# Kernel tuning notes

Hardware: AMD Instinct MI355X
Metric: run time of the kernel (lower is better)

Reference implementation:

```python
import jax, jax.numpy as jnp
import numpy as np

B, L, D = 2, 2048, 2048
H, HKV, HD = 32, 8, 64
G = H // HKV  # GQA group size


def _rope(t, cos, sin):
    # t: [B, h, L, HD]; cos/sin: [L, HD//2]; pairs are consecutive (view_as_complex)
    tr, ti = t[..., 0::2], t[..., 1::2]
    out_r = tr * cos - ti * sin
    out_i = tr * sin + ti * cos
    return jnp.stack([out_r, out_i], axis=-1).reshape(t.shape)


def setup_inputs() -> dict:
    key = jax.random.key(0)
    ks = jax.random.split(key, 5)
    x = jax.random.normal(ks[0], (B, L, D), dtype=jnp.float32)
    wq = jax.random.normal(ks[1], (D, H * HD), dtype=jnp.float32) * 0.02
    wk = jax.random.normal(ks[2], (D, HKV * HD), dtype=jnp.float32) * 0.02
    wv = jax.random.normal(ks[3], (D, HKV * HD), dtype=jnp.float32) * 0.02
    wo = jax.random.normal(ks[4], (D, D), dtype=jnp.float32) * 0.02
    # RoPE freqs: theta_i = 10000^(-2i/HD), angle[p, i] = p * theta_i
    inv_freq = 1.0 / (10000.0 ** (jnp.arange(0, HD, 2, dtype=jnp.float32) / HD))
    angles = jnp.arange(L, dtype=jnp.float32)[:, None] * inv_freq[None, :]  # [L, HD//2]
    freqs_cos = jnp.cos(angles)
    freqs_sin = jnp.sin(angles)
    # additive causal mask [L, L]
    mask = jnp.where(jnp.tril(jnp.ones((L, L), dtype=bool)), 0.0, -1e9).astype(jnp.float32)
    return {"x": x, "wq": wq, "wk": wk, "wv": wv, "wo": wo,
            "freqs_cos": freqs_cos, "freqs_sin": freqs_sin, "mask": mask}


def reference(x, wq, wk, wv, wo, freqs_cos, freqs_sin, mask):
    b, l, _ = x.shape
    q = (x @ wq).reshape(b, l, H, HD).transpose(0, 2, 1, 3)      # [B, H, L, HD]
    k = (x @ wk).reshape(b, l, HKV, HD).transpose(0, 2, 1, 3)    # [B, HKV, L, HD]
    v = (x @ wv).reshape(b, l, HKV, HD).transpose(0, 2, 1, 3)
    q = _rope(q, freqs_cos, freqs_sin)
    k = _rope(k, freqs_cos, freqs_sin)
    # native GQA broadcast instead of repeat_kv copy (same math)
    qg = q.reshape(b, HKV, G, l, HD)
    scores = jnp.einsum("bhgqd,bhkd->bhgqk", qg, k) / jnp.sqrt(jnp.float32(HD))
    scores = scores + mask  # [B, HKV, G, L, L]
    probs = jax.nn.softmax(scores.astype(jnp.float32), axis=-1).astype(v.dtype)
    out = jnp.einsum("bhgqk,bhkd->bhgqd", probs, v)              # [B, HKV, G, L, HD]
    out = out.reshape(b, H, l, HD).transpose(0, 2, 1, 3).reshape(b, l, H * HD)
    return out @ wo
```

## Files before the change

### kernel.cpp

```cpp
#include <hip/hip_runtime.h>
#include <hip/hip_bf16.h>

#define B_   2
#define L_   2048
#define D_   2048
#define H_   32
#define HKV_ 8
#define HD_  64
#define G_   4
#define M_   4096
#define NF_  3072

typedef __attribute__((ext_vector_type(8))) short bf16x8;
typedef __attribute__((ext_vector_type(4))) float f32x4;

static __device__ __forceinline__ unsigned short f2bf(float f) {
  unsigned int u = __float_as_uint(f);
  unsigned int r = (u + 0x7FFFu + ((u >> 16) & 1u)) >> 16;
  return (unsigned short)r;
}
static __device__ __forceinline__ unsigned short f2bf_hw(float f) {
  __hip_bfloat16 h = __float2bfloat16(f);
  return *(unsigned short*)&h;
}

#define GLD16(g, l) __builtin_amdgcn_global_load_lds(                      \
    (const __attribute__((address_space(1))) void*)(g),                    \
    (__attribute__((address_space(3))) void*)(l), 16, 0, 0)

__global__ void cast_bf16_kernel(const float* __restrict__ in,
                                 unsigned short* __restrict__ out, int n4) {
  int i = blockIdx.x * blockDim.x + threadIdx.x;
  if (i >= n4) return;
  float4 v = ((const float4*)in)[i];
  uint2 r;
  r.x = (unsigned int)f2bf(v.x) | ((unsigned int)f2bf(v.y) << 16);
  r.y = (unsigned int)f2bf(v.z) | ((unsigned int)f2bf(v.w) << 16);
  ((uint2*)out)[i] = r;
}

__global__ void transpose_cast_kernel(const float* __restrict__ src,
                                      unsigned short* __restrict__ dst,
                                      int K, int N) {
  __shared__ float tile[32][33];
  int k0 = blockIdx.y * 32, n0 = blockIdx.x * 32;
  int tx = threadIdx.x, ty = threadIdx.y;
#pragma unroll
  for (int r = 0; r < 4; ++r)
    tile[ty * 4 + r][tx] = src[(size_t)(k0 + ty * 4 + r) * N + n0 + tx];
  __syncthreads();
#pragma unroll
  for (int r = 0; r < 4; ++r)
    dst[(size_t)(n0 + ty * 4 + r) * K + k0 + tx] = f2bf(tile[tx][ty * 4 + r]);
}

__global__ __launch_bounds__(256)
void gemm_bt_kernel(const unsigned short* __restrict__ A,
                    const unsigned short* __restrict__ Bt,
                    float* __restrict__ C, int M, int N, int K) {
  __shared__ unsigned short Al[128 * 32];
  __shared__ unsigned short Bl[128 * 32];
  const int tid = threadIdx.x;
  const int w = tid >> 6;
  const int l = tid & 63;
  const int row0 = blockIdx.y * 128;
  const int col0 = blockIdx.x * 128;
  const int wr = (w >> 1) * 64, wc = (w & 1) * 64;

  f32x4 acc[4][4];
#pragma unroll
  for (int m = 0; m < 4; ++m)
#pragma unroll
    for (int n = 0; n < 4; ++n) acc[m][n] = (f32x4){0.f, 0.f, 0.f, 0.f};

  const int srow = l >> 2;
  const int scol = (l & 3) * 8;
  const int fr = l & 15, fk = (l >> 4) * 8;
  const int nk = K / 32;

  for (int kt = 0; kt < nk; ++kt) {
    const int k0 = kt * 32;
#pragma unroll
    for (int t = 0; t < 2; ++t) {
      const int rr = (w * 2 + t) * 16 + srow;
      GLD16(A + (size_t)(row0 + rr) * K + k0 + scol, &Al[(w * 2 + t) * 512]);
      GLD16(Bt + (size_t)(col0 + rr) * K + k0 + scol, &Bl[(w * 2 + t) * 512]);
    }
    __syncthreads();
    bf16x8 af[4], bfr[4];
#pragma unroll
    for (int m = 0; m < 4; ++m)
      af[m] = *(const bf16x8*)&Al[(wr + m * 16 + fr) * 32 + fk];
#pragma unroll
    for (int n = 0; n < 4; ++n)
      bfr[n] = *(const bf16x8*)&Bl[(wc + n * 16 + fr) * 32 + fk];
#pragma unroll
    for (int m = 0; m < 4; ++m)
#pragma unroll
      for (int n = 0; n < 4; ++n)
        acc[m][n] = __builtin_amdgcn_mfma_f32_16x16x32_bf16(af[m], bfr[n], acc[m][n], 0, 0, 0);
    __syncthreads();
  }

  const int fq = l >> 4;
#pragma unroll
  for (int m = 0; m < 4; ++m)
#pragma unroll
    for (int n = 0; n < 4; ++n)
#pragma unroll
      for (int j = 0; j < 4; ++j) {
        int r = row0 + wr + m * 16 + fq * 4 + j;
        int c = col0 + wc + n * 16 + fr;
        C[(size_t)r * N + c] = acc[m][n][j];
      }
}

__global__ void rope_kernel(const float* __restrict__ src,
                            const float* __restrict__ cosf,
                            const float* __restrict__ sinf,
                            unsigned short* __restrict__ dst, int nh, int col_off,
                            float scale, int total) {
  int idx = blockIdx.x * blockDim.x + threadIdx.x;
  if (idx >= total) return;
  int i = idx & 31;
  int h = (idx >> 5) & (nh - 1);
  int row = idx / (nh << 5);
  int lpos = row & (L_ - 1);
  int b = row >> 11;
  const float* s = src + (size_t)row * NF_ + col_off + h * 64 + 2 * i;
  float tr = s[0], ti = s[1];
  float c = cosf[lpos * 32 + i], sn = sinf[lpos * 32 + i];
  float orr = (tr * c - ti * sn) * scale;
  float oii = (tr * sn + ti * c) * scale;
  size_t o = (((size_t)(b * nh + h)) * L_ + lpos) * 64 + 2 * i;
  unsigned int packed = (unsigned int)f2bf(orr) | ((unsigned int)f2bf(oii) << 16);
  *(unsigned int*)&dst[o] = packed;
}

__global__ void cast_vT_kernel(const float* __restrict__ v,
                               unsigned short* __restrict__ vT) {
  __shared__ float tile[32][33];
  int l0 = blockIdx.x * 32, d0 = blockIdx.y * 32;
  int z = blockIdx.z;
  int b = z >> 3, hkv = z & 7;
  int tx = threadIdx.x, ty = threadIdx.y;
  const float* src = v + (size_t)(b * L_) * NF_ + 2560 + hkv * 64;
#pragma unroll
  for (int r = 0; r < 4; ++r)
    tile[ty * 4 + r][tx] = src[(size_t)(l0 + ty * 4 + r) * NF_ + d0 + tx];
  __syncthreads();
  unsigned short* dst = vT + ((size_t)z * 64) * L_;
#pragma unroll
  for (int r = 0; r < 4; ++r)
    dst[(size_t)(d0 + ty * 4 + r) * L_ + l0 + tx] = f2bf(tile[tx][ty * 4 + r]);
}

__global__ __launch_bounds__(256)
void attn_kernel(const unsigned short* __restrict__ Q,
                 const unsigned short* __restrict__ Kt,
                 const unsigned short* __restrict__ Vt,
                 unsigned short* __restrict__ O) {
  __shared__ unsigned short Kl[64 * 64];
  __shared__ unsigned short Vl[64 * 64];
  __shared__ unsigned short Pl[64 * 64];
  const int tid = threadIdx.x, w = tid >> 6, l = tid & 63;
  const int bh = blockIdx.x;
  const int b = bh >> 5, h = bh & 31;
  const int hkv = h >> 2;
  const int pair = blockIdx.y;
  const int fr = l & 15, hi = l >> 4;
  const int frx = fr & 7;

  const int srow = l >> 3;
  const int scole = ((l & 7) ^ srow) * 8;

  const unsigned short* kbase = Kt + ((size_t)(b * HKV_ + hkv)) * L_ * 64;
  const unsigned short* vbase = Vt + ((size_t)(b * HKV_ + hkv)) * 64 * L_;

  for (int half = 0; half < 2; ++half) {
    const int by = half ? (15 - pair) : pair;
    const int q0 = by * 128;

    bf16x8 qf[2][2];
#pragma unroll
    for (int s = 0; s < 2; ++s) {
      const unsigned short* qb =
          Q + (((size_t)bh) * L_ + q0 + s * 64 + w * 16 + fr) * 64 + hi * 8;
      qf[s][0] = *(const bf16x8*)(qb);
      qf[s][1] = *(const bf16x8*)(qb + 32);
    }

    float m_i[2][4], l_p[2][4];
    f32x4 oacc[2][4];
#pragma unroll
    for (int s = 0; s < 2; ++s)
#pragma unroll
      for (int j = 0; j < 4; ++j) { m_i[s][j] = -1e30f; l_p[s][j] = 0.f; }
#pragma unroll
    for (int s = 0; s < 2; ++s)
#pragma unroll
      for (int nf = 0; nf < 4; ++nf) oacc[s][nf] = (f32x4){0.f, 0.f, 0.f, 0.f};

    const int nt = 2 * by + 2;

    for (int t = 0; t < nt; ++t) {
      const int kv0 = t * 64;
#pragma unroll
      for (int u = 0; u < 2; ++u) {
        const int c = w * 2 + u;
        const int rr = c * 8 + srow;
        GLD16(kbase + ((size_t)(kv0 + rr)) * 64 + scole, &Kl[c * 512]);
        GLD16(vbase + ((size_t)rr) * L_ + kv0 + scole, &Vl[c * 512]);
      }
      __syncthreads();

#pragma unroll
      for (int s = 0; s < 2; ++s) {
        const int dlim = 2 * by + s;
        if (t > dlim) continue;

        f32x4 sacc[4];
#pragma unroll
        for (int nf = 0; nf < 4; ++nf) sacc[nf] = (f32x4){0.f, 0.f, 0.f, 0.f};
#pragma unroll
        for (int ks = 0; ks < 2; ++ks) {
#pragma unroll
          for (int nf = 0; nf < 4; ++nf) {
            bf16x8 kfrag = *(const bf16x8*)
                &Kl[(nf * 16 + fr) * 64 + (((ks * 4 + hi) ^ frx) * 8)];
            sacc[nf] = __builtin_amdgcn_mfma_f32_16x16x32_bf16(qf[s][ks], kfrag, sacc[nf], 0, 0, 0);
          }
        }

        if (t == dlim) {
          const int rbase = q0 + s * 64 + w * 16 + hi * 4;
#pragma unroll
          for (int nf = 0; nf < 4; ++nf)
#pragma unroll
            for (int j = 0; j < 4; ++j)
              if (kv0 + nf * 16 + fr > rbase + j) sacc[nf][j] = -1e30f;
        }

        float rowmax[4];
#pragma unroll
        for (int j = 0; j < 4; ++j) {
          float mx = fmaxf(fmaxf(sacc[0][j], sacc[1][j]),
                           fmaxf(sacc[2][j], sacc[3][j]));
          mx = fmaxf(mx, __shfl_xor(mx, 1));
          mx = fmaxf(mx, __shfl_xor(mx, 2));
          mx = fmaxf(mx, __shfl_xor(mx, 4));
          mx = fmaxf(mx, __shfl_xor(mx, 8));
          rowmax[j] = mx;
        }

        float g = rowmax[0] - m_i[s][0];
        g = fmaxf(g, rowmax[1] - m_i[s][1]);
        g = fmaxf(g, rowmax[2] - m_i[s][2]);
        g = fmaxf(g, rowmax[3] - m_i[s][3]);
        if (!__all(g <= 8.f)) {
#pragma unroll
          for (int j = 0; j < 4; ++j) {
            float mnew = fmaxf(m_i[s][j], rowmax[j]);
            float cr = exp2f(m_i[s][j] - mnew);
            m_i[s][j] = mnew;
            l_p[s][j] *= cr;
#pragma unroll
            for (int nf = 0; nf < 4; ++nf) oacc[s][nf][j] *= cr;
          }
        }

#pragma unroll
        for (int j = 0; j < 4; ++j) {
          const int prow = w * 16 + hi * 4 + j;
#pragma unroll
          for (int nf = 0; nf < 4; ++nf) {
            float p = exp2f(sacc[nf][j] - m_i[s][j]);
            l_p[s][j] += p;
            Pl[prow * 64 + (((nf * 2 + (fr >> 3)) ^ (prow & 7)) * 8) + frx] =
                f2bf_hw(p);
          }
        }

#pragma unroll
        for (int ks = 0; ks < 2; ++ks) {
          bf16x8 pa = *(const bf16x8*)
              &Pl[(w * 16 + fr) * 64 + (((ks * 4 + hi) ^ frx) * 8)];
#pragma unroll
          for (int nf = 0; nf < 4; ++nf) {
            bf16x8 vfrag = *(const bf16x8*)
                &Vl[(nf * 16 + fr) * 64 + (((ks * 4 + hi) ^ frx) * 8)];
            oacc[s][nf] = __builtin_amdgcn_mfma_f32_16x16x32_bf16(pa, vfrag, oacc[s][nf], 0, 0, 0);
          }
        }
      }
      __syncthreads();
    }

#pragma unroll
    for (int s = 0; s < 2; ++s)
#pragma unroll
      for (int j = 0; j < 4; ++j) {
        float lsum = l_p[s][j];
        lsum += __shfl_xor(lsum, 1);
        lsum += __shfl_xor(lsum, 2);
        lsum += __shfl_xor(lsum, 4);
        lsum += __shfl_xor(lsum, 8);
        float inv = 1.0f / lsum;
#pragma unroll
        for (int nf = 0; nf < 4; ++nf) {
          int qrow = q0 + s * 64 + w * 16 + hi * 4 + j;
          int d = nf * 16 + fr;
          O[((size_t)(b * L_ + qrow)) * 2048 + h * 64 + d] =
              f2bf_hw(oacc[s][nf][j] * inv);
        }
      }
  }
}

extern "C" void kernel_launch(void* const* d_in, const int* in_sizes, int n_in,
                              void* d_out, int out_size, void* d_ws, size_t ws_size,
                              hipStream_t stream) {
  (void)in_sizes; (void)n_in; (void)out_size; (void)ws_size;
  const float* x  = (const float*)d_in[0];
  const float* wq = (const float*)d_in[1];
  const float* wk = (const float*)d_in[2];
  const float* wv = (const float*)d_in[3];
  const float* wo = (const float*)d_in[4];
  const float* fc = (const float*)d_in[5];
  const float* fs = (const float*)d_in[6];
  float* out = (float*)d_out;

  char* ws = (char*)d_ws;
  unsigned short* x_b  = (unsigned short*)(ws + 0);
  unsigned short* wT   = (unsigned short*)(ws + 16777216);
  unsigned short* woT  = (unsigned short*)(ws + 29360128);
  float* qkv_f         = (float*)(ws + 37748736);
  unsigned short* at_b = (unsigned short*)(ws + 37748736);
  unsigned short* q_b  = (unsigned short*)(ws + 88080384);
  unsigned short* k_b  = (unsigned short*)(ws + 104857600);
  unsigned short* vT_b = (unsigned short*)(ws + 109051904);

  const float qscale = 0.125f * 1.4426950408889634f;

  dim3 tb(32, 8);
  cast_bf16_kernel<<<8192, 256, 0, stream>>>(x, x_b, M_ * D_ / 4);
  transpose_cast_kernel<<<dim3(64, 64), tb, 0, stream>>>(wq, wT, 2048, 2048);
  transpose_cast_kernel<<<dim3(16, 64), tb, 0, stream>>>(wk, wT + (size_t)2048 * 2048, 2048, 512);
  transpose_cast_kernel<<<dim3(16, 64), tb, 0, stream>>>(wv, wT + (size_t)2560 * 2048, 2048, 512);
  transpose_cast_kernel<<<dim3(64, 64), tb, 0, stream>>>(wo, woT, 2048, 2048);

  gemm_bt_kernel<<<dim3(24, 32), 256, 0, stream>>>(x_b, wT, qkv_f, M_, NF_, 2048);

  rope_kernel<<<16384, 256, 0, stream>>>(qkv_f, fc, fs, q_b, 32, 0, qscale, M_ * 32 * 32);
  rope_kernel<<<4096, 256, 0, stream>>>(qkv_f, fc, fs, k_b, 8, 2048, 1.0f, M_ * 8 * 32);
  cast_vT_kernel<<<dim3(64, 2, 16), tb, 0, stream>>>(qkv_f, vT_b);

  attn_kernel<<<dim3(64, 8), 256, 0, stream>>>(q_b, k_b, vT_b, at_b);

  gemm_bt_kernel<<<dim3(16, 32), 256, 0, stream>>>(at_b, woT, out, M_, 2048, 2048);
}
```

Measured before the change: 399.0 us.

## Double-buffer attention K/V tiles, remap blocks, vectorize RoPE kernel

The attention kernel now double-buffers K/V tiles in LDS, issuing the next tile's async loads before computing on the current one and using vmcnt waits with raw barriers. It also drops the paired-half causal balancing in favour of one q-tile per block, with a linear remap of block IDs. MFMA sections are wrapped in s_setprio, and the RoPE kernel now handles 8 elements per thread using float4 loads and uint4 stores. The aim is to hide global load latency and cut per-thread overhead, at the cost of doubling LDS and possible causal load imbalance across blocks.

```diff
diff --git a/kernel.cpp b/kernel.cpp
--- a/kernel.cpp
+++ b/kernel.cpp
@@ -122,19 +122,30 @@
                             float scale, int total) {
   int idx = blockIdx.x * blockDim.x + threadIdx.x;
   if (idx >= total) return;
-  int i = idx & 31;
-  int h = (idx >> 5) & (nh - 1);
-  int row = idx / (nh << 5);
+  int g = idx & 7;
+  int h = (idx >> 3) & (nh - 1);
+  int row = idx / (nh << 3);
   int lpos = row & (L_ - 1);
   int b = row >> 11;
-  const float* s = src + (size_t)row * NF_ + col_off + h * 64 + 2 * i;
-  float tr = s[0], ti = s[1];
-  float c = cosf[lpos * 32 + i], sn = sinf[lpos * 32 + i];
-  float orr = (tr * c - ti * sn) * scale;
-  float oii = (tr * sn + ti * c) * scale;
-  size_t o = (((size_t)(b * nh + h)) * L_ + lpos) * 64 + 2 * i;
-  unsigned int packed = (unsigned int)f2bf(orr) | ((unsigned int)f2bf(oii) << 16);
-  *(unsigned int*)&dst[o] = packed;
+  const float* s = src + (size_t)row * NF_ + col_off + h * 64 + g * 8;
+  float4 v0 = *(const float4*)s;
+  float4 v1 = *(const float4*)(s + 4);
+  float4 c4 = *(const float4*)(cosf + lpos * 32 + g * 4);
+  float4 s4 = *(const float4*)(sinf + lpos * 32 + g * 4);
+  float o0 = (v0.x * c4.x - v0.y * s4.x) * scale;
+  float o1 = (v0.x * s4.x + v0.y * c4.x) * scale;
+  float o2 = (v0.z * c4.y - v0.w * s4.y) * scale;
+  float o3 = (v0.z * s4.y + v0.w * c4.y) * scale;
+  float o4 = (v1.x * c4.z - v1.y * s4.z) * scale;
+  float o5 = (v1.x * s4.z + v1.y * c4.z) * scale;
+  float o6 = (v1.z * c4.w - v1.w * s4.w) * scale;
+  float o7 = (v1.z * s4.w + v1.w * c4.w) * scale;
+  uint4 r;
+  r.x = (unsigned int)f2bf(o0) | ((unsigned int)f2bf(o1) << 16);
+  r.y = (unsigned int)f2bf(o2) | ((unsigned int)f2bf(o3) << 16);
+  r.z = (unsigned int)f2bf(o4) | ((unsigned int)f2bf(o5) << 16);
+  r.w = (unsigned int)f2bf(o6) | ((unsigned int)f2bf(o7) << 16);
+  *(uint4*)&dst[(((size_t)(b * nh + h)) * L_ + lpos) * 64 + g * 8] = r;
 }
 
 __global__ void cast_vT_kernel(const float* __restrict__ v,
@@ -160,14 +171,16 @@
                  const unsigned short* __restrict__ Kt,
                  const unsigned short* __restrict__ Vt,
                  unsigned short* __restrict__ O) {
-  __shared__ unsigned short Kl[64 * 64];
-  __shared__ unsigned short Vl[64 * 64];
+  __shared__ unsigned short Kl[2][64 * 64];
+  __shared__ unsigned short Vl[2][64 * 64];
   __shared__ unsigned short Pl[64 * 64];
   const int tid = threadIdx.x, w = tid >> 6, l = tid & 63;
-  const int bh = blockIdx.x;
+  const int lin = blockIdx.y * 16 + blockIdx.x;
+  const int work = ((lin & 7) << 7) + (lin >> 3);
+  const int bh = work >> 4, by = work & 15;
   const int b = bh >> 5, h = bh & 31;
   const int hkv = h >> 2;
-  const int pair = blockIdx.y;
+  const int q0 = by * 128;
   const int fr = l & 15, hi = l >> 4;
   const int frx = fr & 7;
 
@@ -177,144 +190,158 @@
   const unsigned short* kbase = Kt + ((size_t)(b * HKV_ + hkv)) * L_ * 64;
   const unsigned short* vbase = Vt + ((size_t)(b * HKV_ + hkv)) * 64 * L_;
 
-  for (int half = 0; half < 2; ++half) {
-    const int by = half ? (15 - pair) : pair;
-    const int q0 = by * 128;
-
-    bf16x8 qf[2][2];
+  bf16x8 qf[2][2];
+#pragma unroll
+  for (int s = 0; s < 2; ++s) {
+    const unsigned short* qb =
+        Q + (((size_t)bh) * L_ + q0 + s * 64 + w * 16 + fr) * 64 + hi * 8;
+    qf[s][0] = *(const bf16x8*)(qb);
+    qf[s][1] = *(const bf16x8*)(qb + 32);
+  }
+
+  float m_i[2][4], l_p[2][4];
+  f32x4 oacc[2][4];
+#pragma unroll
+  for (int s = 0; s < 2; ++s)
+#pragma unroll
+    for (int j = 0; j < 4; ++j) { m_i[s][j] = -1e30f; l_p[s][j] = 0.f; }
+#pragma unroll
+  for (int s = 0; s < 2; ++s)
+#pragma unroll
+    for (int nf = 0; nf < 4; ++nf) oacc[s][nf] = (f32x4){0.f, 0.f, 0.f, 0.f};
+
+  const int nt = 2 * by + 2;
+
+#define ASTAGE(kv0_, buf_) do {                                              \
+    _Pragma("unroll")                                                        \
+    for (int u_ = 0; u_ < 2; ++u_) {                                         \
+      const int c_ = w * 2 + u_;                                             \
+      const int rr_ = c_ * 8 + srow;                                         \
+      GLD16(kbase + ((size_t)((kv0_) + rr_)) * 64 + scole,                   \
+            &Kl[buf_][c_ * 512]);                                            \
+      GLD16(vbase + ((size_t)rr_) * L_ + (kv0_) + scole,                     \
+            &Vl[buf_][c_ * 512]);                                            \
+    }                                                                        \
+  } while (0)
+
+  ASTAGE(0, 0);
+
+  for (int t = 0; t < nt; ++t) {
+    const int buf = t & 1;
+    if (t + 1 < nt) {
+      ASTAGE((t + 1) * 64, buf ^ 1);
+      asm volatile("s_waitcnt vmcnt(4)" ::: "memory");
+    } else {
+      asm volatile("s_waitcnt vmcnt(0)" ::: "memory");
+    }
+    __builtin_amdgcn_s_barrier();
+
+    const int kv0 = t * 64;
 #pragma unroll
     for (int s = 0; s < 2; ++s) {
-      const unsigned short* qb =
-          Q + (((size_t)bh) * L_ + q0 + s * 64 + w * 16 + fr) * 64 + hi * 8;
-      qf[s][0] = *(const bf16x8*)(qb);
-      qf[s][1] = *(const bf16x8*)(qb + 32);
+      const int dlim = 2 * by + s;
+      if (t > dlim) continue;
+
+      f32x4 sacc[4];
+#pragma unroll
+      for (int nf = 0; nf < 4; ++nf) sacc[nf] = (f32x4){0.f, 0.f, 0.f, 0.f};
+      __builtin_amdgcn_s_setprio(1);
+#pragma unroll
+      for (int ks = 0; ks < 2; ++ks) {
+#pragma unroll
+        for (int nf = 0; nf < 4; ++nf) {
+          bf16x8 kfrag = *(const bf16x8*)
+              &Kl[buf][(nf * 16 + fr) * 64 + (((ks * 4 + hi) ^ frx) * 8)];
+          sacc[nf] = __builtin_amdgcn_mfma_f32_16x16x32_bf16(qf[s][ks], kfrag, sacc[nf], 0, 0, 0);
+        }
+      }
+      __builtin_amdgcn_s_setprio(0);
+
+      if (t == dlim) {
+        const int rbase = q0 + s * 64 + w * 16 + hi * 4;
+#pragma unroll
+        for (int nf = 0; nf < 4; ++nf)
+#pragma unroll
+          for (int j = 0; j < 4; ++j)
+            if (kv0 + nf * 16 + fr > rbase + j) sacc[nf][j] = -1e30f;
+      }
+
+      float rowmax[4];
+#pragma unroll
+      for (int j = 0; j < 4; ++j) {
+        float mx = fmaxf(fmaxf(sacc[0][j], sacc[1][j]),
+                         fmaxf(sacc[2][j], sacc[3][j]));
+        mx = fmaxf(mx, __shfl_xor(mx, 1));
+        mx = fmaxf(mx, __shfl_xor(mx, 2));
+        mx = fmaxf(mx, __shfl_xor(mx, 4));
+        mx = fmaxf(mx, __shfl_xor(mx, 8));
+        rowmax[j] = mx;
+      }
+
+      float g = rowmax[0] - m_i[s][0];
+      g = fmaxf(g, rowmax[1] - m_i[s][1]);
+      g = fmaxf(g, rowmax[2] - m_i[s][2]);
+      g = fmaxf(g, rowmax[3] - m_i[s][3]);
+      if (!__all(g <= 8.f)) {
+#pragma unroll
+        for (int j = 0; j < 4; ++j) {
+          float mnew = fmaxf(m_i[s][j], rowmax[j]);
+          float cr = exp2f(m_i[s][j] - mnew);
+          m_i[s][j] = mnew;
+          l_p[s][j] *= cr;
+#pragma unroll
+          for (int nf = 0; nf < 4; ++nf) oacc[s][nf][j] *= cr;
+        }
+      }
+
+#pragma unroll
+      for (int j = 0; j < 4; ++j) {
+        const int prow = w * 16 + hi * 4 + j;
+#pragma unroll
+        for (int nf = 0; nf < 4; ++nf) {
+          float p = exp2f(sacc[nf][j] - m_i[s][j]);
+          l_p[s][j] += p;
+          Pl[prow * 64 + (((nf * 2 + (fr >> 3)) ^ (prow & 7)) * 8) + frx] =
+              f2bf_hw(p);
+        }
+      }
+
+      __builtin_amdgcn_s_setprio(1);
+#pragma unroll
+      for (int ks = 0; ks < 2; ++ks) {
+        bf16x8 pa = *(const bf16x8*)
+            &Pl[(w * 16 + fr) * 64 + (((ks * 4 + hi) ^ frx) * 8)];
+#pragma unroll
+        for (int nf = 0; nf < 4; ++nf) {
+          bf16x8 vfrag = *(const bf16x8*)
+              &Vl[buf][(nf * 16 + fr) * 64 + (((ks * 4 + hi) ^ frx) * 8)];
+          oacc[s][nf] = __builtin_amdgcn_mfma_f32_16x16x32_bf16(pa, vfrag, oacc[s][nf], 0, 0, 0);
+        }
+      }
+      __builtin_amdgcn_s_setprio(0);
     }
-
-    float m_i[2][4], l_p[2][4];
-    f32x4 oacc[2][4];
-#pragma unroll
-    for (int s = 0; s < 2; ++s)
-#pragma unroll
-      for (int j = 0; j < 4; ++j) { m_i[s][j] = -1e30f; l_p[s][j] = 0.f; }
-#pragma unroll
-    for (int s = 0; s < 2; ++s)
-#pragma unroll
-      for (int nf = 0; nf < 4; ++nf) oacc[s][nf] = (f32x4){0.f, 0.f, 0.f, 0.f};
-
-    const int nt = 2 * by + 2;
-
-    for (int t = 0; t < nt; ++t) {
-      const int kv0 = t * 64;
-#pragma unroll
-      for (int u = 0; u < 2; ++u) {
-        const int c = w * 2 + u;
-        const int rr = c * 8 + srow;
-        GLD16(kbase + ((size_t)(kv0 + rr)) * 64 + scole, &Kl[c * 512]);
-        GLD16(vbase + ((size_t)rr) * L_ + kv0 + scole, &Vl[c * 512]);
-      }
-      __syncthreads();
-
-#pragma unroll
-      for (int s = 0; s < 2; ++s) {
-        const int dlim = 2 * by + s;
-        if (t > dlim) continue;
-
-        f32x4 sacc[4];
-#pragma unroll
-        for (int nf = 0; nf < 4; ++nf) sacc[nf] = (f32x4){0.f, 0.f, 0.f, 0.f};
-#pragma unroll
-        for (int ks = 0; ks < 2; ++ks) {
-#pragma unroll
-          for (int nf = 0; nf < 4; ++nf) {
-            bf16x8 kfrag = *(const bf16x8*)
-                &Kl[(nf * 16 + fr) * 64 + (((ks * 4 + hi) ^ frx) * 8)];
-            sacc[nf] = __builtin_amdgcn_mfma_f32_16x16x32_bf16(qf[s][ks], kfrag, sacc[nf], 0, 0, 0);
-          }
-        }
-
-        if (t == dlim) {
-          const int rbase = q0 + s * 64 + w * 16 + hi * 4;
-#pragma unroll
-          for (int nf = 0; nf < 4; ++nf)
-#pragma unroll
-            for (int j = 0; j < 4; ++j)
-              if (kv0 + nf * 16 + fr > rbase + j) sacc[nf][j] = -1e30f;
-        }
-
-        float rowmax[4];
-#pragma unroll
-        for (int j = 0; j < 4; ++j) {
-          float mx = fmaxf(fmaxf(sacc[0][j], sacc[1][j]),
-                           fmaxf(sacc[2][j], sacc[3][j]));
-          mx = fmaxf(mx, __shfl_xor(mx, 1));
-          mx = fmaxf(mx, __shfl_xor(mx, 2));
-          mx = fmaxf(mx, __shfl_xor(mx, 4));
-          mx = fmaxf(mx, __shfl_xor(mx, 8));
-          rowmax[j] = mx;
-        }
-
-        float g = rowmax[0] - m_i[s][0];
-        g = fmaxf(g, rowmax[1] - m_i[s][1]);
-        g = fmaxf(g, rowmax[2] - m_i[s][2]);
-        g = fmaxf(g, rowmax[3] - m_i[s][3]);
-        if (!__all(g <= 8.f)) {
-#pragma unroll
-          for (int j = 0; j < 4; ++j) {
-            float mnew = fmaxf(m_i[s][j], rowmax[j]);
-            float cr = exp2f(m_i[s][j] - mnew);
-            m_i[s][j] = mnew;
-            l_p[s][j] *= cr;
-#pragma unroll
-            for (int nf = 0; nf < 4; ++nf) oacc[s][nf][j] *= cr;
-          }
-        }
-
-#pragma unroll
-        for (int j = 0; j < 4; ++j) {
-          const int prow = w * 16 + hi * 4 + j;
-#pragma unroll
-          for (int nf = 0; nf < 4; ++nf) {
-            float p = exp2f(sacc[nf][j] - m_i[s][j]);
-            l_p[s][j] += p;
-            Pl[prow * 64 + (((nf * 2 + (fr >> 3)) ^ (prow & 7)) * 8) + frx] =
-                f2bf_hw(p);
-          }
-        }
-
-#pragma unroll
-        for (int ks = 0; ks < 2; ++ks) {
-          bf16x8 pa = *(const bf16x8*)
-              &Pl[(w * 16 + fr) * 64 + (((ks * 4 + hi) ^ frx) * 8)];
-#pragma unroll
-          for (int nf = 0; nf < 4; ++nf) {
-            bf16x8 vfrag = *(const bf16x8*)
-                &Vl[(nf * 16 + fr) * 64 + (((ks * 4 + hi) ^ frx) * 8)];
-            oacc[s][nf] = __builtin_amdgcn_mfma_f32_16x16x32_bf16(pa, vfrag, oacc[s][nf], 0, 0, 0);
-          }
-        }
-      }
-      __syncthreads();
+    __builtin_amdgcn_s_barrier();
+  }
+#undef ASTAGE
+
+#pragma unroll
+  for (int s = 0; s < 2; ++s)
+#pragma unroll
+    for (int j = 0; j < 4; ++j) {
+      float lsum = l_p[s][j];
+      lsum += __shfl_xor(lsum, 1);
+      lsum += __shfl_xor(lsum, 2);
+      lsum += __shfl_xor(lsum, 4);
+      lsum += __shfl_xor(lsum, 8);
+      float inv = 1.0f / lsum;
+#pragma unroll
+      for (int nf = 0; nf < 4; ++nf) {
+        int qrow = q0 + s * 64 + w * 16 + hi * 4 + j;
+        int d = nf * 16 + fr;
+        O[((size_t)(b * L_ + qrow)) * 2048 + h * 64 + d] =
+            f2bf_hw(oacc[s][nf][j] * inv);
+      }
     }
-
-#pragma unroll
-    for (int s = 0; s < 2; ++s)
-#pragma unroll
-      for (int j = 0; j < 4; ++j) {
-        float lsum = l_p[s][j];
-        lsum += __shfl_xor(lsum, 1);
-        lsum += __shfl_xor(lsum, 2);
-        lsum += __shfl_xor(lsum, 4);
-        lsum += __shfl_xor(lsum, 8);
-        float inv = 1.0f / lsum;
-#pragma unroll
-        for (int nf = 0; nf < 4; ++nf) {
-          int qrow = q0 + s * 64 + w * 16 + hi * 4 + j;
-          int d = nf * 16 + fr;
-          O[((size_t)(b * L_ + qrow)) * 2048 + h * 64 + d] =
-              f2bf_hw(oacc[s][nf][j] * inv);
-        }
-      }
-  }
 }
 
 extern "C" void kernel_launch(void* const* d_in, const int* in_sizes, int n_in,
@@ -351,11 +378,11 @@
 
   gemm_bt_kernel<<<dim3(24, 32), 256, 0, stream>>>(x_b, wT, qkv_f, M_, NF_, 2048);
 
-  rope_kernel<<<16384, 256, 0, stream>>>(qkv_f, fc, fs, q_b, 32, 0, qscale, M_ * 32 * 32);
-  rope_kernel<<<4096, 256, 0, stream>>>(qkv_f, fc, fs, k_b, 8, 2048, 1.0f, M_ * 8 * 32);
+  rope_kernel<<<4096, 256, 0, stream>>>(qkv_f, fc, fs, q_b, 32, 0, qscale, M_ * 32 * 8);
+  rope_kernel<<<1024, 256, 0, stream>>>(qkv_f, fc, fs, k_b, 8, 2048, 1.0f, M_ * 8 * 8);
   cast_vT_kernel<<<dim3(64, 2, 16), tb, 0, stream>>>(qkv_f, vT_b);
 
-  attn_kernel<<<dim3(64, 8), 256, 0, stream>>>(q_b, k_b, vT_b, at_b);
+  attn_kernel<<<dim3(16, 64), 256, 0, stream>>>(q_b, k_b, vT_b, at_b);
 
   gemm_bt_kernel<<<dim3(16, 32), 256, 0, stream>>>(at_b, woT, out, M_, 2048, 2048);
 }
```

Result: slower. 449.4 us (+12.6%).
